# Kernel optimization log

Hardware: AMD Instinct MI355X
Metric: run time of the kernel (lower is better)

## Reference

```python
import jax, jax.numpy as jnp
import numpy as np

D_MODEL = 192
NODE_NUM = 64
DEPTH = 2
ALPHA = 0.05
NUM_LAYERS = 2
LN_EPS = 1e-5


def _gcn(x, p):
    # x: [N, in_dim*D_MODEL]; faithful port of GCN.forward (eval mode)
    nv1, nv2, ws, bs, wm, bm, we, be, wl, bl, g, b = p
    N = x.shape[0]
    in_dim = x.shape[1] // D_MODEL
    adp = jax.nn.softmax(jax.nn.relu(nv1 @ nv2), axis=1)            # [V,V]
    adj = adp + jnp.eye(NODE_NUM, dtype=x.dtype)
    a = adj / adj.sum(1, keepdims=True)                              # row-normalized
    h0 = jax.lax.conv_general_dilated(
        x.reshape(N, in_dim, D_MODEL), ws, (1,), 'VALID',
        dimension_numbers=('NCH', 'OIH', 'NCH')) + bs[None, :, None]  # [N,C,V]
    h = h0
    outs = [h0]
    for _ in range(DEPTH):
        h = ALPHA * h0 + (1.0 - ALPHA) * jnp.einsum('ncw,vw->ncv', h, a)
        outs.append(h)
    ho = jnp.concatenate(outs, axis=1)                               # [N,(DEPTH+1)C,V]
    ho = jax.nn.gelu(jnp.einsum('ncv,oc->nov', ho, wm) + bm[None, :, None], approximate=False)
    ho = jnp.einsum('ncv,oc->nov', ho, we) + be[None, :, None]       # [N,6,V]
    ho = jnp.einsum('nov,dv->nod', ho, wl) + bl                      # [N,6,D]
    mu = ho.mean(-1, keepdims=True)
    var = ((ho - mu) ** 2).mean(-1, keepdims=True)                   # biased, like torch LN
    ho = (ho - mu) / jnp.sqrt(var + LN_EPS) * g + b
    return ho.reshape(N, 6 * D_MODEL)


def _encoder(inp4, flag, layer_params):
    x = jnp.transpose(inp4, (2, 0, 1, 3)) if flag == 1 else jnp.transpose(inp4, (1, 0, 2, 3))
    W, B, O, D = x.shape
    L = W + O - 1
    N = W * B
    # input_transfer: shift row r by r along the slice axis
    place = jax.vmap(lambda xr, r: jax.lax.dynamic_update_slice(
        jnp.zeros((B, L, D), x.dtype), xr, (0, r, 0)))
    a = place(x, jnp.arange(W)).reshape(N, L, D)
    layer0_output = None
    output_all = None
    rows_layers, cols_layers = [], []
    for layer in range(NUM_LAYERS):
        if layer >= 1:
            a = output_all  # eval mode: F.dropout is identity
            if layer == 1:
                layer0_output = a
        p = layer_params[layer]

        def step(carry, x_t, p=p):
            h_row, h_col = carry
            gate = _gcn(jnp.concatenate([h_row, h_col, x_t], axis=-1), p)  # [N,6D]
            sg = jax.nn.sigmoid(gate[:, :4 * D])
            tg = jnp.tanh(gate[:, 4 * D:])
            ug_r, og_r, ug_c, og_c = jnp.split(sg, 4, axis=-1)
            ig_r, ig_c = jnp.split(tg, 2, axis=-1)
            h_row = jnp.tanh((1.0 - ug_r) * h_row + ug_r * ig_r) * og_r
            h_col = jnp.tanh((1.0 - ug_c) * h_col + ug_c * ig_c) * og_c
            out_s = jnp.concatenate([h_row, h_col], axis=-1)
            # col hidden is saved pre-roll, rolled for next step
            return (h_row, jnp.roll(h_col, B, axis=0)), (out_s, h_row, h_col)

        init = (jnp.zeros((N, D), x.dtype), jnp.zeros((N, D), x.dtype))
        _, (outs, hrows, hcols) = jax.lax.scan(step, init, jnp.swapaxes(a, 0, 1))
        output_all = jnp.swapaxes(outs, 0, 1)                        # [N,L,2D]
        if layer >= 1:
            output_all = output_all + layer0_output
        # rows saved at slice s>=O-1 from block loc = s-O+1
        rows = hrows.reshape(L, W, B, D)[jnp.arange(O - 1, L), jnp.arange(W)]  # [W,B,D]
        # cols saved at slice s>=W-1 from last batch block
        cols = hcols[W - 1:, (W - 1) * B:, :]                        # [O,B,D]
        rows_layers.append(rows)
        cols_layers.append(cols)
    hidden_row_all = jnp.stack(rows_layers).transpose(2, 0, 1, 3)    # [B,layers,W,D]
    hidden_col_all = jnp.stack(cols_layers).transpose(2, 0, 1, 3)    # [B,layers,O,D]
    if flag == 1:
        return output_all, hidden_col_all, hidden_row_all
    return output_all, hidden_row_all, hidden_col_all


def setup_inputs() -> dict:
    key = jax.random.key(0)
    ks = jax.random.split(key, 20)
    idx = [0]
    def nxt():
        k = ks[idx[0]]
        idx[0] += 1
        return k
    B, W, O = 8, 24, 48
    K = D_MODEL - NODE_NUM + 1  # 129
    cc, sc, nd = 16, 32, 40
    d = {"input": jax.random.normal(nxt(), (B, W, O, D_MODEL), dtype=jnp.float32)}
    for li, in_dim in enumerate([3, 4]):
        d[f"nodevec1_{li}"] = jax.random.normal(nxt(), (NODE_NUM, nd), dtype=jnp.float32)
        d[f"nodevec2_{li}"] = jax.random.normal(nxt(), (nd, NODE_NUM), dtype=jnp.float32)
        d[f"w_start_{li}"] = jax.random.normal(nxt(), (cc, in_dim, K), dtype=jnp.float32) * 0.05
        d[f"b_start_{li}"] = jnp.zeros((cc,), jnp.float32)
        d[f"w_mlp_{li}"] = jax.random.normal(nxt(), (sc, (DEPTH + 1) * cc), dtype=jnp.float32) * 0.05
        d[f"b_mlp_{li}"] = jnp.zeros((sc,), jnp.float32)
        d[f"w_end_{li}"] = jax.random.normal(nxt(), (6, sc), dtype=jnp.float32) * 0.05
        d[f"b_end_{li}"] = jnp.zeros((6,), jnp.float32)
        d[f"w_lin_{li}"] = jax.random.normal(nxt(), (D_MODEL, NODE_NUM), dtype=jnp.float32) * 0.05
        d[f"b_lin_{li}"] = jnp.zeros((D_MODEL,), jnp.float32)
        d[f"gamma_{li}"] = jnp.ones((D_MODEL,), jnp.float32)
        d[f"beta_{li}"] = jnp.zeros((D_MODEL,), jnp.float32)
    d["flag"] = 0
    return d


def reference(input, nodevec1_0, nodevec2_0, w_start_0, b_start_0, w_mlp_0, b_mlp_0,
              w_end_0, b_end_0, w_lin_0, b_lin_0, gamma_0, beta_0,
              nodevec1_1, nodevec2_1, w_start_1, b_start_1, w_mlp_1, b_mlp_1,
              w_end_1, b_end_1, w_lin_1, b_lin_1, gamma_1, beta_1, flag):
    p0 = (nodevec1_0, nodevec2_0, w_start_0, b_start_0, w_mlp_0, b_mlp_0,
          w_end_0, b_end_0, w_lin_0, b_lin_0, gamma_0, beta_0)
    p1 = (nodevec1_1, nodevec2_1, w_start_1, b_start_1, w_mlp_1, b_mlp_1,
          w_end_1, b_end_1, w_lin_1, b_lin_1, gamma_1, beta_1)
    return _encoder(input, flag, (p0, p1))
```

## Files before the change

### kernel.cpp

```cpp
#include <hip/hip_runtime.h>
#include <hip/hip_bf16.h>

#define NT 256
typedef unsigned short u16;

__device__ __forceinline__ u16 tobf(float x) {
  union { __hip_bfloat16 h; u16 u; } cv;
  cv.h = __float2bfloat16(x);
  return cv.u;
}
__device__ __forceinline__ float frombf(u16 u) {
  return __uint_as_float(((unsigned)u) << 16);
}
__device__ __forceinline__ float sigf(float x) {
  return __builtin_amdgcn_rcpf(1.f + __builtin_amdgcn_exp2f(-1.4426950408889634f * x));
}
__device__ __forceinline__ float tanh_fast(float x) {
  return 1.f - 2.f * __builtin_amdgcn_rcpf(1.f + __builtin_amdgcn_exp2f(2.8853900817779268f * x));
}

struct SeqArgs {
  const float* input;
  const float* nv1_0; const float* nv2_0; const float* nv1_1; const float* nv2_1;
  const float* w_start0; const float* b_start0; const float* w_mlp0; const float* b_mlp0;
  const float* w_end0;   const float* b_end0;   const float* w_lin0; const float* b_lin0;
  const float* gamma0;   const float* beta0;
  const float* w_start1; const float* b_start1; const float* w_mlp1; const float* b_mlp1;
  const float* w_end1;   const float* b_end1;   const float* w_lin1; const float* b_lin1;
  const float* gamma1;   const float* beta1;
  float* HCOL;
  int*   flags;
  float* out_all; float* out_hrow; float* out_hcol;
};

__global__ __launch_bounds__(NT, 1) void seq_kernel(SeqArgs A) {
  const int n = blockIdx.x, w = n >> 3, b = n & 7, tid = threadIdx.x;
  const int pred = (n + 184) % 192;

  __shared__ __align__(16) float sCIN[768];
  __shared__ __align__(16) u16   sWS[64 * 132];
  __shared__ __align__(16) float sAT[4096];
  __shared__ __align__(16) float sH[2][1024];
  __shared__ __align__(16) float sAbuf[4928];
  float* const sPart = sAbuf;
  float* const sG    = sAbuf;
  float* const sE    = sAbuf + 2048;
  float* const sY    = sAbuf;
  float* const smWE  = sAbuf + 3072;
  float* const smBE  = sAbuf + 3264;
  float* const smWM  = sAbuf + 3328;

  for (int layer = 0; layer < 2; ++layer) {
    const int in_dim = 3 + layer;
    const int P = in_dim - 1;
    const float* nv1    = layer ? A.nv1_1    : A.nv1_0;
    const float* nv2    = layer ? A.nv2_1    : A.nv2_0;
    const float* wstart = layer ? A.w_start1 : A.w_start0;
    const float* bs     = layer ? A.b_start1 : A.b_start0;
    const float* wm     = layer ? A.w_mlp1   : A.w_mlp0;
    const float* bm     = layer ? A.b_mlp1   : A.b_mlp0;
    const float* we     = layer ? A.w_end1   : A.w_end0;
    const float* be     = layer ? A.b_end1   : A.b_end0;
    const float* wl     = layer ? A.w_lin1   : A.w_lin0;
    const float* bl     = layer ? A.b_lin1   : A.b_lin0;
    const float* gm     = layer ? A.gamma1   : A.gamma0;
    const float* bt     = layer ? A.beta1    : A.beta0;

    for (int idx = tid; idx < 4096; idx += NT) {
      int v = idx >> 6, ww = idx & 63;
      float s = 0.f;
      for (int j = 0; j < 40; ++j) s = fmaf(nv1[v*40 + j], nv2[j*64 + ww], s);
      sAbuf[idx] = fmaxf(s, 0.f);
    }
    __syncthreads();
    if (tid < 64) {
      const int v = tid;
      float m = -1e30f;
      for (int ww = 0; ww < 64; ++ww) m = fmaxf(m, sAbuf[v*64 + ww]);
      float s = 0.f;
      for (int ww = 0; ww < 64; ++ww) { float e = expf(sAbuf[v*64 + ww] - m); sAbuf[v*64 + ww] = e; s += e; }
      float inv = 1.f / s, rs = 1.f;
      for (int ww = 0; ww < 64; ++ww) rs += sAbuf[v*64 + ww] * inv;
      float irs = 1.f / rs;
      for (int ww = 0; ww < 64; ++ww) {
        float a = sAbuf[v*64 + ww] * inv + ((ww == v) ? 1.f : 0.f);
        sAT[ww*64 + v] = a * irs;
      }
    }
    __syncthreads();
    for (int idx = tid; idx < 16*in_dim*132; idx += NT) {
      int row = idx / 132, k = idx - row*132;
      sWS[idx] = (k < 129) ? tobf(wstart[((row & 15)*in_dim + (row >> 4))*129 + k]) : (u16)0;
    }
    for (int idx = tid; idx < 1536; idx += NT) { int o = idx/48, c = idx - o*48; smWM[o*50 + c] = wm[idx]; }
    for (int idx = tid; idx < 192; idx += NT) smWE[idx] = we[idx];
    if (tid < 6) smBE[tid] = be[tid];
    for (int d = tid; d < 384; d += NT) sCIN[d] = 0.f;

    const int o_m = tid >> 3, v8 = (tid & 7)*8;
    const int v_p = tid & 63, cq = tid >> 6;
    const float bmv = bm[o_m];
    float blv = 0.f, gmv = 1.f, btv = 0.f;
    if (tid < 192) { blv = bl[tid]; gmv = gm[tid]; btv = bt[tid]; }
    float bs_r[4];
#pragma unroll
    for (int m = 0; m < 4; ++m) bs_r[m] = bs[(tid >> 6) + 4*m];
    __syncthreads();

    auto pre_phase = [&](int t) {
      if (layer == 0) {
        int o = t - w;
        if (o >= 0 && o < 48) {
          const float* xr = A.input + (((size_t)(b*24 + w)*48 + o)*192);
          for (int d = tid; d < 192; d += NT) sCIN[384 + d] = xr[d];
        } else {
          for (int d = tid; d < 192; d += NT) sCIN[384 + d] = 0.f;
        }
      } else {
        const float* xr = A.out_all + ((size_t)n*71 + t)*384;
        for (int d = tid; d < 384; d += NT) sCIN[384 + d] = xr[d];
      }
      __syncthreads();
      {
        const int ci = tid >> 2, vq = tid & 3;
        const int p = ci >> 4, c = ci & 15;
        if (p < P) {
          const int ich = (p == 0) ? 0 : (p + 1);
          float acc[16];
#pragma unroll
          for (int j = 0; j < 16; ++j) acc[j] = 0.f;
          const float* xin = (p == 0) ? &sCIN[vq*16] : &sCIN[384 + (p-1)*192 + vq*16];
          const u16* wrow = &sWS[(ich*16 + c)*132];
          for (int k4 = 0; k4 < 128; k4 += 4) {
            ushort4 wu = *(const ushort4*)(wrow + k4);
            float w0 = frombf(wu.x), w1 = frombf(wu.y), w2 = frombf(wu.z), w3 = frombf(wu.w);
            union { float4 v4[5]; float f[20]; } X;
#pragma unroll
            for (int m = 0; m < 5; ++m) X.v4[m] = *(const float4*)(xin + k4 + 4*m);
#pragma unroll
            for (int j = 0; j < 16; ++j) {
              acc[j] = fmaf(w0, X.f[j],   acc[j]);
              acc[j] = fmaf(w1, X.f[j+1], acc[j]);
              acc[j] = fmaf(w2, X.f[j+2], acc[j]);
              acc[j] = fmaf(w3, X.f[j+3], acc[j]);
            }
          }
          {
            float wk = frombf(wrow[128]);
            union { float4 v4[4]; float f[16]; } X;
#pragma unroll
            for (int m = 0; m < 4; ++m) X.v4[m] = *(const float4*)(xin + 128 + 4*m);
#pragma unroll
            for (int j = 0; j < 16; ++j) acc[j] = fmaf(wk, X.f[j], acc[j]);
          }
          float* pp = &sPart[(p*16 + c)*64 + vq*16];
#pragma unroll
          for (int m = 0; m < 4; ++m)
            *(float4*)(pp + 4*m) = make_float4(acc[4*m], acc[4*m+1], acc[4*m+2], acc[4*m+3]);
        }
      }
      __syncthreads();
      {
        int m = 0;
        for (int idx = tid; idx < 1024; idx += NT, ++m) {
          int c = idx >> 6, v = idx & 63;
          float s = bs_r[m];
          for (int p = 0; p < P; ++p) s += sPart[(p*16 + c)*64 + v];
          sH[0][idx] = s;
        }
      }
      __syncthreads();
    };
    pre_phase(0);

    for (int t = 0; t < 71; ++t) {
      const int S = layer*71 + t;

      if (t > 0) {
        if (tid == 0) {
          while (__hip_atomic_load(&A.flags[pred*32], __ATOMIC_ACQUIRE, __HIP_MEMORY_SCOPE_AGENT) < S)
            __builtin_amdgcn_s_sleep(1);
        }
        __syncthreads();
        float* hc = A.HCOL + ((size_t)((S-1) & 31)*192 + pred)*192;
        for (int d = tid; d < 192; d += NT)
          sCIN[192 + d] = __hip_atomic_load(&hc[d], __ATOMIC_RELAXED, __HIP_MEMORY_SCOPE_AGENT);
        __syncthreads();
      }

      {
        const int c = tid >> 4, vg = tid & 15;
        const float* xin = &sCIN[192 + vg*4];
        const u16* wrow = &sWS[(16 + c)*132];
        float4 a4 = *(const float4*)&sH[0][c*64 + vg*4];
        float a0 = a4.x, a1 = a4.y, a2 = a4.z, a3 = a4.w;
        float4 xc = *(const float4*)xin;
        for (int k4 = 0; k4 < 128; k4 += 4) {
          ushort4 wu = *(const ushort4*)(wrow + k4);
          float w0 = frombf(wu.x), w1 = frombf(wu.y), w2 = frombf(wu.z), w3 = frombf(wu.w);
          float4 xn = *(const float4*)(xin + k4 + 4);
          a0 = fmaf(w3, xc.w, fmaf(w2, xc.z, fmaf(w1, xc.y, fmaf(w0, xc.x, a0))));
          a1 = fmaf(w3, xn.x, fmaf(w2, xc.w, fmaf(w1, xc.z, fmaf(w0, xc.y, a1))));
          a2 = fmaf(w3, xn.y, fmaf(w2, xn.x, fmaf(w1, xc.w, fmaf(w0, xc.z, a2))));
          a3 = fmaf(w3, xn.z, fmaf(w2, xn.y, fmaf(w1, xn.x, fmaf(w0, xc.w, a3))));
          xc = xn;
        }
        float wk = frombf(wrow[128]);
        a0 = fmaf(wk, xc.x, a0); a1 = fmaf(wk, xc.y, a1);
        a2 = fmaf(wk, xc.z, a2); a3 = fmaf(wk, xc.w, a3);
        *(float4*)&sH[0][c*64 + vg*4] = make_float4(a0, a1, a2, a3);
      }
      __syncthreads();

      float g[8];
      {
#pragma unroll
        for (int j = 0; j < 8; ++j) g[j] = bmv;
        float pa[4] = {0.f, 0.f, 0.f, 0.f};
        for (int w4 = 0; w4 < 64; w4 += 4) {
          float a0 = sAT[(w4+0)*64 + v_p];
          float a1 = sAT[(w4+1)*64 + v_p];
          float a2 = sAT[(w4+2)*64 + v_p];
          float a3 = sAT[(w4+3)*64 + v_p];
#pragma unroll
          for (int j = 0; j < 4; ++j) {
            float4 h = *(const float4*)&sH[0][(cq*4 + j)*64 + w4];
            pa[j] = fmaf(h.x, a0, pa[j]); pa[j] = fmaf(h.y, a1, pa[j]);
            pa[j] = fmaf(h.z, a2, pa[j]); pa[j] = fmaf(h.w, a3, pa[j]);
          }
        }
#pragma unroll
        for (int j = 0; j < 4; ++j) {
          int c = cq*4 + j;
          sH[1][c*64 + v_p] = fmaf(0.95f, pa[j], 0.05f*sH[0][c*64 + v_p]);
        }
        for (int c = 0; c < 16; ++c) {
          float wv = smWM[o_m*50 + c];
          float4 ha = *(const float4*)&sH[0][c*64 + v8];
          float4 hb = *(const float4*)&sH[0][c*64 + v8 + 4];
          g[0]=fmaf(wv,ha.x,g[0]); g[1]=fmaf(wv,ha.y,g[1]); g[2]=fmaf(wv,ha.z,g[2]); g[3]=fmaf(wv,ha.w,g[3]);
          g[4]=fmaf(wv,hb.x,g[4]); g[5]=fmaf(wv,hb.y,g[5]); g[6]=fmaf(wv,hb.z,g[6]); g[7]=fmaf(wv,hb.w,g[7]);
        }
      }
      __syncthreads();

      {
        float pa[4] = {0.f, 0.f, 0.f, 0.f};
        for (int w4 = 0; w4 < 64; w4 += 4) {
          float a0 = sAT[(w4+0)*64 + v_p];
          float a1 = sAT[(w4+1)*64 + v_p];
          float a2 = sAT[(w4+2)*64 + v_p];
          float a3 = sAT[(w4+3)*64 + v_p];
#pragma unroll
          for (int j = 0; j < 4; ++j) {
            float4 h = *(const float4*)&sH[1][(cq*4 + j)*64 + w4];
            pa[j] = fmaf(h.x, a0, pa[j]); pa[j] = fmaf(h.y, a1, pa[j]);
            pa[j] = fmaf(h.z, a2, pa[j]); pa[j] = fmaf(h.w, a3, pa[j]);
          }
        }
#pragma unroll
        for (int j = 0; j < 4; ++j) {
          int c = cq*4 + j;
          float h0v = sH[0][c*64 + v_p];
          sH[0][c*64 + v_p] = fmaf(0.95f, pa[j], 0.05f*h0v);
        }
        for (int c = 0; c < 16; ++c) {
          float wv = smWM[o_m*50 + 16 + c];
          float4 ha = *(const float4*)&sH[1][c*64 + v8];
          float4 hb = *(const float4*)&sH[1][c*64 + v8 + 4];
          g[0]=fmaf(wv,ha.x,g[0]); g[1]=fmaf(wv,ha.y,g[1]); g[2]=fmaf(wv,ha.z,g[2]); g[3]=fmaf(wv,ha.w,g[3]);
          g[4]=fmaf(wv,hb.x,g[4]); g[5]=fmaf(wv,hb.y,g[5]); g[6]=fmaf(wv,hb.z,g[6]); g[7]=fmaf(wv,hb.w,g[7]);
        }
      }
      __syncthreads();

      {
        for (int c = 0; c < 16; ++c) {
          float wv = smWM[o_m*50 + 32 + c];
          float4 ha = *(const float4*)&sH[0][c*64 + v8];
          float4 hb = *(const float4*)&sH[0][c*64 + v8 + 4];
          g[0]=fmaf(wv,ha.x,g[0]); g[1]=fmaf(wv,ha.y,g[1]); g[2]=fmaf(wv,ha.z,g[2]); g[3]=fmaf(wv,ha.w,g[3]);
          g[4]=fmaf(wv,hb.x,g[4]); g[5]=fmaf(wv,hb.y,g[5]); g[6]=fmaf(wv,hb.z,g[6]); g[7]=fmaf(wv,hb.w,g[7]);
        }
#pragma unroll
        for (int j = 0; j < 8; ++j) {
          float x = g[j];
          g[j] = 0.5f * x * (1.f + erff(x * 0.70710678118654752f));
        }
        *(float4*)&sG[o_m*64 + v8]     = make_float4(g[0], g[1], g[2], g[3]);
        *(float4*)&sG[o_m*64 + v8 + 4] = make_float4(g[4], g[5], g[6], g[7]);
      }
      __syncthreads();

      for (int idx = tid; idx < 384; idx += NT) {
        int o2 = idx >> 6, v = idx & 63;
        float acc = smBE[o2];
        for (int c = 0; c < 32; ++c) acc = fmaf(smWE[o2*32 + c], sG[c*64 + v], acc);
        sE[idx] = acc;
      }
      __syncthreads();

      if (tid < 192) {
        const int d = tid;
        const float4* wrow = (const float4*)(wl + d*64);
        float y0=blv, y1=blv, y2=blv, y3=blv, y4=blv, y5=blv;
        for (int q = 0; q < 16; ++q) {
          float4 wv = wrow[q];
          float4 e0 = *(const float4*)&sE[0*64 + q*4];
          float4 e1 = *(const float4*)&sE[1*64 + q*4];
          float4 e2 = *(const float4*)&sE[2*64 + q*4];
          float4 e3 = *(const float4*)&sE[3*64 + q*4];
          float4 e4 = *(const float4*)&sE[4*64 + q*4];
          float4 e5 = *(const float4*)&sE[5*64 + q*4];
          y0 = fmaf(e0.x,wv.x, fmaf(e0.y,wv.y, fmaf(e0.z,wv.z, fmaf(e0.w,wv.w, y0))));
          y1 = fmaf(e1.x,wv.x, fmaf(e1.y,wv.y, fmaf(e1.z,wv.z, fmaf(e1.w,wv.w, y1))));
          y2 = fmaf(e2.x,wv.x, fmaf(e2.y,wv.y, fmaf(e2.z,wv.z, fmaf(e2.w,wv.w, y2))));
          y3 = fmaf(e3.x,wv.x, fmaf(e3.y,wv.y, fmaf(e3.z,wv.z, fmaf(e3.w,wv.w, y3))));
          y4 = fmaf(e4.x,wv.x, fmaf(e4.y,wv.y, fmaf(e4.z,wv.z, fmaf(e4.w,wv.w, y4))));
          y5 = fmaf(e5.x,wv.x, fmaf(e5.y,wv.y, fmaf(e5.z,wv.z, fmaf(e5.w,wv.w, y5))));
        }
        sY[0*192+d]=y0; sY[1*192+d]=y1; sY[2*192+d]=y2;
        sY[3*192+d]=y3; sY[4*192+d]=y4; sY[5*192+d]=y5;
      }
      __syncthreads();

      if (tid < 192) {
        const int r = tid >> 5, l32 = tid & 31;
        float sm = 0.f, sq = 0.f;
#pragma unroll
        for (int m = 0; m < 6; ++m) {
          float v = sY[r*192 + l32 + 32*m];
          sm += v; sq = fmaf(v, v, sq);
        }
#pragma unroll
        for (int off = 16; off >= 1; off >>= 1) {
          sm += __shfl_xor(sm, off);
          sq += __shfl_xor(sq, off);
        }
        if (l32 == 0) {
          float mu = sm * (1.f/192.f);
          float var = sq * (1.f/192.f) - mu*mu;
          sH[1][r] = mu;
          sH[1][8 + r] = rsqrtf(fmaxf(var, 0.f) + 1e-5f);
        }
      }
      __syncthreads();

      float hcn = 0.f;
      if (tid < 192) {
        const int d = tid;
        float y2 = fmaf((sY[2*192+d] - sH[1][2]) * sH[1][10], gmv, btv);
        float y3 = fmaf((sY[3*192+d] - sH[1][3]) * sH[1][11], gmv, btv);
        float y5 = fmaf((sY[5*192+d] - sH[1][5]) * sH[1][13], gmv, btv);
        float ugc = sigf(y2), ogc = sigf(y3), igc = tanh_fast(y5);
        float hc = sCIN[192 + d];
        hcn = tanh_fast(fmaf(ugc, igc, (1.f - ugc)*hc)) * ogc;
        __hip_atomic_store(&A.HCOL[((size_t)(S & 31)*192 + n)*192 + d], hcn,
                           __ATOMIC_RELAXED, __HIP_MEMORY_SCOPE_AGENT);
      }
      __syncthreads();
      if (tid == 0) {
        __threadfence();
        __hip_atomic_store(&A.flags[n*32], S + 1, __ATOMIC_RELEASE, __HIP_MEMORY_SCOPE_AGENT);
      }
      if (tid < 192) {
        const int d = tid;
        float y0 = fmaf((sY[0*192+d] - sH[1][0]) * sH[1][8],  gmv, btv);
        float y1 = fmaf((sY[1*192+d] - sH[1][1]) * sH[1][9],  gmv, btv);
        float y4 = fmaf((sY[4*192+d] - sH[1][4]) * sH[1][12], gmv, btv);
        float ugr = sigf(y0), ogr = sigf(y1), igr = tanh_fast(y4);
        float hr = sCIN[d];
        float hrn = tanh_fast(fmaf(ugr, igr, (1.f - ugr)*hr)) * ogr;
        sCIN[d] = hrn;
        float* oa = A.out_all + ((size_t)n*71 + t)*384;
        if (layer == 0) { oa[d] = hrn; oa[192 + d] = hcn; }
        else           { oa[d] = hrn + sCIN[384 + d]; oa[192 + d] = hcn + sCIN[576 + d]; }
        if (t == 47 + w)
          A.out_hrow[(((size_t)b*2 + layer)*24 + w)*192 + d] = hrn;
        if (w == 23 && t >= 23)
          A.out_hcol[(((size_t)b*2 + layer)*48 + (t - 23))*192 + d] = hcn;
      }
      __syncthreads();
      if (t < 70) pre_phase(t + 1);
    }
    __syncthreads();
  }
}

extern "C" void kernel_launch(void* const* d_in, const int* in_sizes, int n_in,
                              void* d_out, int out_size, void* d_ws, size_t ws_size,
                              hipStream_t stream) {
  (void)in_sizes; (void)n_in; (void)out_size; (void)ws_size;
  char* ws = (char*)d_ws;
  int*   flags = (int*)ws;
  float* HCOL  = (float*)(ws + 24576);

  hipMemsetAsync(flags, 0, 24576, stream);

  SeqArgs A;
  A.input    = (const float*)d_in[0];
  A.nv1_0    = (const float*)d_in[1];  A.nv2_0 = (const float*)d_in[2];
  A.w_start0 = (const float*)d_in[3];  A.b_start0 = (const float*)d_in[4];
  A.w_mlp0   = (const float*)d_in[5];  A.b_mlp0   = (const float*)d_in[6];
  A.w_end0   = (const float*)d_in[7];  A.b_end0   = (const float*)d_in[8];
  A.w_lin0   = (const float*)d_in[9];  A.b_lin0   = (const float*)d_in[10];
  A.gamma0   = (const float*)d_in[11]; A.beta0    = (const float*)d_in[12];
  A.nv1_1    = (const float*)d_in[13]; A.nv2_1 = (const float*)d_in[14];
  A.w_start1 = (const float*)d_in[15]; A.b_start1 = (const float*)d_in[16];
  A.w_mlp1   = (const float*)d_in[17]; A.b_mlp1   = (const float*)d_in[18];
  A.w_end1   = (const float*)d_in[19]; A.b_end1   = (const float*)d_in[20];
  A.w_lin1   = (const float*)d_in[21]; A.b_lin1   = (const float*)d_in[22];
  A.gamma1   = (const float*)d_in[23]; A.beta1    = (const float*)d_in[24];
  A.HCOL = HCOL; A.flags = flags;
  A.out_all  = (float*)d_out;
  A.out_hrow = (float*)d_out + 5234688;
  A.out_hcol = (float*)d_out + 5308416;

  seq_kernel<<<192, NT, 0, stream>>>(A);
}
```

Measured before the change: 2.878 ms.

## Double block threads to 512 and repartition per-step GCN work across threads

Raises the block size from 256 to 512 threads and redistributes every phase of the per-timestep GCN (start conv, graph propagation, MLP, linear projection) so each thread computes fewer outputs. The aim is to shorten the serial latency of each recurrent step in this latency-bound, flag-synchronised sequential kernel by exposing more parallelism per block. In exchange there are more waves for each __syncthreads, lower per-thread ILP, and possibly less efficient LDS access patterns (scalar instead of float4 loads).

```diff
diff --git a/kernel.cpp b/kernel.cpp
--- a/kernel.cpp
+++ b/kernel.cpp
@@ -1,7 +1,7 @@
 #include <hip/hip_runtime.h>
 #include <hip/hip_bf16.h>
 
-#define NT 256
+#define NT 512
 typedef unsigned short u16;
 
 __device__ __forceinline__ u16 tobf(float x) {
@@ -33,7 +33,7 @@
   float* out_all; float* out_hrow; float* out_hcol;
 };
 
-__global__ __launch_bounds__(NT, 1) void seq_kernel(SeqArgs A) {
+__global__ __launch_bounds__(NT, 2) void seq_kernel(SeqArgs A) {
   const int n = blockIdx.x, w = n >> 3, b = n & 7, tid = threadIdx.x;
   const int pred = (n + 184) % 192;
 
@@ -97,14 +97,15 @@
     if (tid < 6) smBE[tid] = be[tid];
     for (int d = tid; d < 384; d += NT) sCIN[d] = 0.f;
 
-    const int o_m = tid >> 3, v8 = (tid & 7)*8;
-    const int v_p = tid & 63, cq = tid >> 6;
-    const float bmv = bm[o_m];
+    const int v_p = tid & 63;
+    const int o0  = tid >> 6;
+    const float bmv0 = bm[o0], bmv1 = bm[o0 + 8], bmv2 = bm[o0 + 16], bmv3 = bm[o0 + 24];
     float blv = 0.f, gmv = 1.f, btv = 0.f;
-    if (tid < 192) { blv = bl[tid]; gmv = gm[tid]; btv = bt[tid]; }
-    float bs_r[4];
-#pragma unroll
-    for (int m = 0; m < 4; ++m) bs_r[m] = bs[(tid >> 6) + 4*m];
+    if (tid < 384) blv = bl[(tid >= 192) ? tid - 192 : tid];
+    if (tid < 192) { gmv = gm[tid]; btv = bt[tid]; }
+    float bs_r[2];
+    bs_r[0] = bs[tid >> 6];
+    bs_r[1] = bs[(tid >> 6) + 8];
     __syncthreads();
 
     auto pre_phase = [&](int t) {
@@ -121,79 +122,15 @@
         for (int d = tid; d < 384; d += NT) sCIN[384 + d] = xr[d];
       }
       __syncthreads();
-      {
-        const int ci = tid >> 2, vq = tid & 3;
-        const int p = ci >> 4, c = ci & 15;
-        if (p < P) {
-          const int ich = (p == 0) ? 0 : (p + 1);
-          float acc[16];
-#pragma unroll
-          for (int j = 0; j < 16; ++j) acc[j] = 0.f;
-          const float* xin = (p == 0) ? &sCIN[vq*16] : &sCIN[384 + (p-1)*192 + vq*16];
-          const u16* wrow = &sWS[(ich*16 + c)*132];
-          for (int k4 = 0; k4 < 128; k4 += 4) {
-            ushort4 wu = *(const ushort4*)(wrow + k4);
-            float w0 = frombf(wu.x), w1 = frombf(wu.y), w2 = frombf(wu.z), w3 = frombf(wu.w);
-            union { float4 v4[5]; float f[20]; } X;
-#pragma unroll
-            for (int m = 0; m < 5; ++m) X.v4[m] = *(const float4*)(xin + k4 + 4*m);
-#pragma unroll
-            for (int j = 0; j < 16; ++j) {
-              acc[j] = fmaf(w0, X.f[j],   acc[j]);
-              acc[j] = fmaf(w1, X.f[j+1], acc[j]);
-              acc[j] = fmaf(w2, X.f[j+2], acc[j]);
-              acc[j] = fmaf(w3, X.f[j+3], acc[j]);
-            }
-          }
-          {
-            float wk = frombf(wrow[128]);
-            union { float4 v4[4]; float f[16]; } X;
-#pragma unroll
-            for (int m = 0; m < 4; ++m) X.v4[m] = *(const float4*)(xin + 128 + 4*m);
-#pragma unroll
-            for (int j = 0; j < 16; ++j) acc[j] = fmaf(wk, X.f[j], acc[j]);
-          }
-          float* pp = &sPart[(p*16 + c)*64 + vq*16];
-#pragma unroll
-          for (int m = 0; m < 4; ++m)
-            *(float4*)(pp + 4*m) = make_float4(acc[4*m], acc[4*m+1], acc[4*m+2], acc[4*m+3]);
-        }
-      }
-      __syncthreads();
-      {
-        int m = 0;
-        for (int idx = tid; idx < 1024; idx += NT, ++m) {
-          int c = idx >> 6, v = idx & 63;
-          float s = bs_r[m];
-          for (int p = 0; p < P; ++p) s += sPart[(p*16 + c)*64 + v];
-          sH[0][idx] = s;
-        }
-      }
-      __syncthreads();
-    };
-    pre_phase(0);
-
-    for (int t = 0; t < 71; ++t) {
-      const int S = layer*71 + t;
-
-      if (t > 0) {
-        if (tid == 0) {
-          while (__hip_atomic_load(&A.flags[pred*32], __ATOMIC_ACQUIRE, __HIP_MEMORY_SCOPE_AGENT) < S)
-            __builtin_amdgcn_s_sleep(1);
-        }
-        __syncthreads();
-        float* hc = A.HCOL + ((size_t)((S-1) & 31)*192 + pred)*192;
-        for (int d = tid; d < 192; d += NT)
-          sCIN[192 + d] = __hip_atomic_load(&hc[d], __ATOMIC_RELAXED, __HIP_MEMORY_SCOPE_AGENT);
-        __syncthreads();
-      }
-
-      {
-        const int c = tid >> 4, vg = tid & 15;
-        const float* xin = &sCIN[192 + vg*4];
-        const u16* wrow = &sWS[(16 + c)*132];
-        float4 a4 = *(const float4*)&sH[0][c*64 + vg*4];
-        float a0 = a4.x, a1 = a4.y, a2 = a4.z, a3 = a4.w;
+      const int nslots = P << 8;
+      for (int s = tid; s < nslots; s += NT) {
+        const int cidx = s >> 4;
+        const int p = cidx >> 4, c = cidx & 15;
+        const int vg = s & 15;
+        const int ich = (p == 0) ? 0 : (p + 1);
+        const float* xin = ((p == 0) ? &sCIN[0] : &sCIN[384 + (p-1)*192]) + vg*4;
+        const u16* wrow = &sWS[(ich*16 + c)*132];
+        float a0 = 0.f, a1 = 0.f, a2 = 0.f, a3 = 0.f;
         float4 xc = *(const float4*)xin;
         for (int k4 = 0; k4 < 128; k4 += 4) {
           ushort4 wu = *(const ushort4*)(wrow + k4);
@@ -208,87 +145,132 @@
         float wk = frombf(wrow[128]);
         a0 = fmaf(wk, xc.x, a0); a1 = fmaf(wk, xc.y, a1);
         a2 = fmaf(wk, xc.z, a2); a3 = fmaf(wk, xc.w, a3);
-        *(float4*)&sH[0][c*64 + vg*4] = make_float4(a0, a1, a2, a3);
-      }
-      __syncthreads();
-
-      float g[8];
-      {
-#pragma unroll
-        for (int j = 0; j < 8; ++j) g[j] = bmv;
-        float pa[4] = {0.f, 0.f, 0.f, 0.f};
+        *(float4*)&sPart[cidx*64 + vg*4] = make_float4(a0, a1, a2, a3);
+      }
+      __syncthreads();
+      {
+        const int c0 = tid >> 6, v = tid & 63;
+        float sum0 = bs_r[0], sum1 = bs_r[1];
+        for (int p = 0; p < P; ++p) {
+          sum0 += sPart[(p*16 + c0     )*64 + v];
+          sum1 += sPart[(p*16 + c0 + 8 )*64 + v];
+        }
+        sH[0][ c0      *64 + v] = sum0;
+        sH[0][(c0 + 8 )*64 + v] = sum1;
+      }
+      __syncthreads();
+    };
+    pre_phase(0);
+
+    for (int t = 0; t < 71; ++t) {
+      const int S = layer*71 + t;
+
+      if (t > 0) {
+        if (tid == 0) {
+          while (__hip_atomic_load(&A.flags[pred*32], __ATOMIC_ACQUIRE, __HIP_MEMORY_SCOPE_AGENT) < S)
+            __builtin_amdgcn_s_sleep(1);
+        }
+        __syncthreads();
+        float* hc = A.HCOL + ((size_t)((S-1) & 31)*192 + pred)*192;
+        for (int d = tid; d < 192; d += NT)
+          sCIN[192 + d] = __hip_atomic_load(&hc[d], __ATOMIC_RELAXED, __HIP_MEMORY_SCOPE_AGENT);
+        __syncthreads();
+      }
+
+      {
+        const int c = tid >> 5, vg2 = tid & 31;
+        const int vbase = c*64 + vg2*2;
+        const float* xin = &sCIN[192 + vg2*2];
+        const u16* wrow = &sWS[(16 + c)*132];
+        float a0 = sH[0][vbase], a1 = sH[0][vbase + 1];
+        float2 xc = *(const float2*)xin;
+        for (int k2 = 0; k2 < 128; k2 += 2) {
+          ushort2 wu = *(const ushort2*)(wrow + k2);
+          float w0 = frombf(wu.x), w1 = frombf(wu.y);
+          float2 xn = *(const float2*)(xin + k2 + 2);
+          a0 = fmaf(w1, xc.y, fmaf(w0, xc.x, a0));
+          a1 = fmaf(w1, xn.x, fmaf(w0, xc.y, a1));
+          xc = xn;
+        }
+        float wk = frombf(wrow[128]);
+        a0 = fmaf(wk, xc.x, a0); a1 = fmaf(wk, xc.y, a1);
+        sH[0][vbase] = a0; sH[0][vbase + 1] = a1;
+      }
+      __syncthreads();
+
+      float g0 = bmv0, g1 = bmv1, g2 = bmv2, g3 = bmv3;
+      {
+        const int c0 = o0 * 2;
+        float pa0 = 0.f, pa1 = 0.f;
         for (int w4 = 0; w4 < 64; w4 += 4) {
-          float a0 = sAT[(w4+0)*64 + v_p];
-          float a1 = sAT[(w4+1)*64 + v_p];
-          float a2 = sAT[(w4+2)*64 + v_p];
-          float a3 = sAT[(w4+3)*64 + v_p];
-#pragma unroll
-          for (int j = 0; j < 4; ++j) {
-            float4 h = *(const float4*)&sH[0][(cq*4 + j)*64 + w4];
-            pa[j] = fmaf(h.x, a0, pa[j]); pa[j] = fmaf(h.y, a1, pa[j]);
-            pa[j] = fmaf(h.z, a2, pa[j]); pa[j] = fmaf(h.w, a3, pa[j]);
-          }
-        }
-#pragma unroll
-        for (int j = 0; j < 4; ++j) {
-          int c = cq*4 + j;
-          sH[1][c*64 + v_p] = fmaf(0.95f, pa[j], 0.05f*sH[0][c*64 + v_p]);
-        }
+          float a0v = sAT[(w4+0)*64 + v_p];
+          float a1v = sAT[(w4+1)*64 + v_p];
+          float a2v = sAT[(w4+2)*64 + v_p];
+          float a3v = sAT[(w4+3)*64 + v_p];
+          float4 h0v = *(const float4*)&sH[0][ c0      *64 + w4];
+          float4 h1v = *(const float4*)&sH[0][(c0 + 1 )*64 + w4];
+          pa0 = fmaf(h0v.x, a0v, pa0); pa0 = fmaf(h0v.y, a1v, pa0);
+          pa0 = fmaf(h0v.z, a2v, pa0); pa0 = fmaf(h0v.w, a3v, pa0);
+          pa1 = fmaf(h1v.x, a0v, pa1); pa1 = fmaf(h1v.y, a1v, pa1);
+          pa1 = fmaf(h1v.z, a2v, pa1); pa1 = fmaf(h1v.w, a3v, pa1);
+        }
+        sH[1][ c0      *64 + v_p] = fmaf(0.95f, pa0, 0.05f * sH[0][ c0      *64 + v_p]);
+        sH[1][(c0 + 1 )*64 + v_p] = fmaf(0.95f, pa1, 0.05f * sH[0][(c0 + 1 )*64 + v_p]);
         for (int c = 0; c < 16; ++c) {
-          float wv = smWM[o_m*50 + c];
-          float4 ha = *(const float4*)&sH[0][c*64 + v8];
-          float4 hb = *(const float4*)&sH[0][c*64 + v8 + 4];
-          g[0]=fmaf(wv,ha.x,g[0]); g[1]=fmaf(wv,ha.y,g[1]); g[2]=fmaf(wv,ha.z,g[2]); g[3]=fmaf(wv,ha.w,g[3]);
-          g[4]=fmaf(wv,hb.x,g[4]); g[5]=fmaf(wv,hb.y,g[5]); g[6]=fmaf(wv,hb.z,g[6]); g[7]=fmaf(wv,hb.w,g[7]);
-        }
-      }
-      __syncthreads();
-
-      {
-        float pa[4] = {0.f, 0.f, 0.f, 0.f};
+          float hv = sH[0][c*64 + v_p];
+          g0 = fmaf(smWM[(o0     )*50 + c], hv, g0);
+          g1 = fmaf(smWM[(o0 +  8)*50 + c], hv, g1);
+          g2 = fmaf(smWM[(o0 + 16)*50 + c], hv, g2);
+          g3 = fmaf(smWM[(o0 + 24)*50 + c], hv, g3);
+        }
+      }
+      __syncthreads();
+
+      {
+        const int c0 = o0 * 2;
+        float pa0 = 0.f, pa1 = 0.f;
         for (int w4 = 0; w4 < 64; w4 += 4) {
-          float a0 = sAT[(w4+0)*64 + v_p];
-          float a1 = sAT[(w4+1)*64 + v_p];
-          float a2 = sAT[(w4+2)*64 + v_p];
-          float a3 = sAT[(w4+3)*64 + v_p];
-#pragma unroll
-          for (int j = 0; j < 4; ++j) {
-            float4 h = *(const float4*)&sH[1][(cq*4 + j)*64 + w4];
-            pa[j] = fmaf(h.x, a0, pa[j]); pa[j] = fmaf(h.y, a1, pa[j]);
-            pa[j] = fmaf(h.z, a2, pa[j]); pa[j] = fmaf(h.w, a3, pa[j]);
-          }
-        }
-#pragma unroll
-        for (int j = 0; j < 4; ++j) {
-          int c = cq*4 + j;
-          float h0v = sH[0][c*64 + v_p];
-          sH[0][c*64 + v_p] = fmaf(0.95f, pa[j], 0.05f*h0v);
-        }
+          float a0v = sAT[(w4+0)*64 + v_p];
+          float a1v = sAT[(w4+1)*64 + v_p];
+          float a2v = sAT[(w4+2)*64 + v_p];
+          float a3v = sAT[(w4+3)*64 + v_p];
+          float4 h0v = *(const float4*)&sH[1][ c0      *64 + w4];
+          float4 h1v = *(const float4*)&sH[1][(c0 + 1 )*64 + w4];
+          pa0 = fmaf(h0v.x, a0v, pa0); pa0 = fmaf(h0v.y, a1v, pa0);
+          pa0 = fmaf(h0v.z, a2v, pa0); pa0 = fmaf(h0v.w, a3v, pa0);
+          pa1 = fmaf(h1v.x, a0v, pa1); pa1 = fmaf(h1v.y, a1v, pa1);
+          pa1 = fmaf(h1v.z, a2v, pa1); pa1 = fmaf(h1v.w, a3v, pa1);
+        }
+        float h00 = sH[0][ c0      *64 + v_p];
+        float h01 = sH[0][(c0 + 1 )*64 + v_p];
+        sH[0][ c0      *64 + v_p] = fmaf(0.95f, pa0, 0.05f * h00);
+        sH[0][(c0 + 1 )*64 + v_p] = fmaf(0.95f, pa1, 0.05f * h01);
         for (int c = 0; c < 16; ++c) {
-          float wv = smWM[o_m*50 + 16 + c];
-          float4 ha = *(const float4*)&sH[1][c*64 + v8];
-          float4 hb = *(const float4*)&sH[1][c*64 + v8 + 4];
-          g[0]=fmaf(wv,ha.x,g[0]); g[1]=fmaf(wv,ha.y,g[1]); g[2]=fmaf(wv,ha.z,g[2]); g[3]=fmaf(wv,ha.w,g[3]);
-          g[4]=fmaf(wv,hb.x,g[4]); g[5]=fmaf(wv,hb.y,g[5]); g[6]=fmaf(wv,hb.z,g[6]); g[7]=fmaf(wv,hb.w,g[7]);
+          float hv = sH[1][c*64 + v_p];
+          g0 = fmaf(smWM[(o0     )*50 + 16 + c], hv, g0);
+          g1 = fmaf(smWM[(o0 +  8)*50 + 16 + c], hv, g1);
+          g2 = fmaf(smWM[(o0 + 16)*50 + 16 + c], hv, g2);
+          g3 = fmaf(smWM[(o0 + 24)*50 + 16 + c], hv, g3);
         }
       }
       __syncthreads();
 
       {
         for (int c = 0; c < 16; ++c) {
-          float wv = smWM[o_m*50 + 32 + c];
-          float4 ha = *(const float4*)&sH[0][c*64 + v8];
-          float4 hb = *(const float4*)&sH[0][c*64 + v8 + 4];
-          g[0]=fmaf(wv,ha.x,g[0]); g[1]=fmaf(wv,ha.y,g[1]); g[2]=fmaf(wv,ha.z,g[2]); g[3]=fmaf(wv,ha.w,g[3]);
-          g[4]=fmaf(wv,hb.x,g[4]); g[5]=fmaf(wv,hb.y,g[5]); g[6]=fmaf(wv,hb.z,g[6]); g[7]=fmaf(wv,hb.w,g[7]);
-        }
-#pragma unroll
-        for (int j = 0; j < 8; ++j) {
-          float x = g[j];
-          g[j] = 0.5f * x * (1.f + erff(x * 0.70710678118654752f));
-        }
-        *(float4*)&sG[o_m*64 + v8]     = make_float4(g[0], g[1], g[2], g[3]);
-        *(float4*)&sG[o_m*64 + v8 + 4] = make_float4(g[4], g[5], g[6], g[7]);
+          float hv = sH[0][c*64 + v_p];
+          g0 = fmaf(smWM[(o0     )*50 + 32 + c], hv, g0);
+          g1 = fmaf(smWM[(o0 +  8)*50 + 32 + c], hv, g1);
+          g2 = fmaf(smWM[(o0 + 16)*50 + 32 + c], hv, g2);
+          g3 = fmaf(smWM[(o0 + 24)*50 + 32 + c], hv, g3);
+        }
+        g0 = 0.5f * g0 * (1.f + erff(g0 * 0.70710678118654752f));
+        g1 = 0.5f * g1 * (1.f + erff(g1 * 0.70710678118654752f));
+        g2 = 0.5f * g2 * (1.f + erff(g2 * 0.70710678118654752f));
+        g3 = 0.5f * g3 * (1.f + erff(g3 * 0.70710678118654752f));
+        sG[(o0     )*64 + v_p] = g0;
+        sG[(o0 +  8)*64 + v_p] = g1;
+        sG[(o0 + 16)*64 + v_p] = g2;
+        sG[(o0 + 24)*64 + v_p] = g3;
       }
       __syncthreads();
 
@@ -300,27 +282,23 @@
       }
       __syncthreads();
 
-      if (tid < 192) {
-        const int d = tid;
+      if (tid < 384) {
+        const int d  = (tid >= 192) ? tid - 192 : tid;
+        const int r0 = (tid >= 192) ? 3 : 0;
         const float4* wrow = (const float4*)(wl + d*64);
-        float y0=blv, y1=blv, y2=blv, y3=blv, y4=blv, y5=blv;
+        float y0 = blv, y1 = blv, y2 = blv;
         for (int q = 0; q < 16; ++q) {
           float4 wv = wrow[q];
-          float4 e0 = *(const float4*)&sE[0*64 + q*4];
-          float4 e1 = *(const float4*)&sE[1*64 + q*4];
-          float4 e2 = *(const float4*)&sE[2*64 + q*4];
-          float4 e3 = *(const float4*)&sE[3*64 + q*4];
-          float4 e4 = *(const float4*)&sE[4*64 + q*4];
-          float4 e5 = *(const float4*)&sE[5*64 + q*4];
+          float4 e0 = *(const float4*)&sE[(r0+0)*64 + q*4];
+          float4 e1 = *(const float4*)&sE[(r0+1)*64 + q*4];
+          float4 e2 = *(const float4*)&sE[(r0+2)*64 + q*4];
           y0 = fmaf(e0.x,wv.x, fmaf(e0.y,wv.y, fmaf(e0.z,wv.z, fmaf(e0.w,wv.w, y0))));
           y1 = fmaf(e1.x,wv.x, fmaf(e1.y,wv.y, fmaf(e1.z,wv.z, fmaf(e1.w,wv.w, y1))));
           y2 = fmaf(e2.x,wv.x, fmaf(e2.y,wv.y, fmaf(e2.z,wv.z, fmaf(e2.w,wv.w, y2))));
-          y3 = fmaf(e3.x,wv.x, fmaf(e3.y,wv.y, fmaf(e3.z,wv.z, fmaf(e3.w,wv.w, y3))));
-          y4 = fmaf(e4.x,wv.x, fmaf(e4.y,wv.y, fmaf(e4.z,wv.z, fmaf(e4.w,wv.w, y4))));
-          y5 = fmaf(e5.x,wv.x, fmaf(e5.y,wv.y, fmaf(e5.z,wv.z, fmaf(e5.w,wv.w, y5))));
-        }
-        sY[0*192+d]=y0; sY[1*192+d]=y1; sY[2*192+d]=y2;
-        sY[3*192+d]=y3; sY[4*192+d]=y4; sY[5*192+d]=y5;
+        }
+        sY[(r0+0)*192 + d] = y0;
+        sY[(r0+1)*192 + d] = y1;
+        sY[(r0+2)*192 + d] = y2;
       }
       __syncthreads();
 
```

New measurement: 2.739 ms. 4.8% less time.
